# Kernel optimization log

Measured on AMD Instinct MI355X. Metric: run time of the kernel, lower is better.

Reference implementation:

```python
import jax, jax.numpy as jnp
import numpy as np

CHUNK = 1024
HEAD_DIM = 128

def setup_inputs() -> dict:
    key = jax.random.key(0)
    k1, k2, k3 = jax.random.split(key, 3)
    B, H, S, D = 2, 16, 4096, HEAD_DIM
    q = jax.random.normal(k1, (B, H, S, D), dtype=jnp.float32)
    k = jax.random.normal(k2, (B, H, S, D), dtype=jnp.float32)
    v = jax.random.normal(k3, (B, H, S, D), dtype=jnp.float32)
    return {"q": q, "k": k, "v": v}

def reference(q, k, v):
    # Faithful to the torch module INCLUDING its masking bug: for every chunk
    # the triu mask uses diagonal=1 in chunk-local coordinates, so chunk-local
    # query row i attends only keys j<=i, i.e. only the first CHUNK keys matter.
    B, H, S, D = q.shape
    scale = D ** (-0.5)
    n = S // CHUNK
    qc = q.reshape(B, H, n, CHUNK, D)           # [B,H,n,C,D]
    kc = k[:, :, :CHUNK, :]                      # [B,H,C,D]
    vc = v[:, :, :CHUNK, :]                      # [B,H,C,D]
    scores = jnp.einsum('bhnid,bhjd->bhnij', qc, kc) * scale  # [B,H,n,C,C]
    mask = jnp.triu(jnp.ones((CHUNK, CHUNK), dtype=bool), 1)   # j > i masked
    scores = jnp.where(mask, -jnp.inf, scores)
    probs = jax.nn.softmax(scores, axis=-1)
    out = jnp.einsum('bhnij,bhjd->bhnid', probs, vc)
    return out.reshape(B, H, S, D)
```

## Files before the change

kernel.cpp:

```cpp
#include <hip/hip_runtime.h>


typedef __attribute__((ext_vector_type(8))) short bfrag_t;
typedef __attribute__((ext_vector_type(16))) float f32x16;
typedef unsigned short u16;
typedef unsigned int   u32;

#define SEQ     4096
#define SCHUNK  1024
#define HD      128
#define NTILE   16
#define TILE_E  8192

__device__ __forceinline__ u16 f2bf(float f) {
    union { float f; unsigned u; } x; x.f = f;
    unsigned r = x.u + 0x7fffu + ((x.u >> 16) & 1u);
    return (u16)(r >> 16);
}

__global__ __launch_bounds__(256)
void mea_prep(const float* __restrict__ kg, const float* __restrict__ vg,
              u16* __restrict__ wsK, u16* __restrict__ wsV)
{
    const int tid  = threadIdx.x;
    const int tile = blockIdx.x;
    const int bh = tile >> 4, kt = tile & 15;
    const long gsrc = (long)bh * SEQ * HD + (long)kt * 64 * HD;
    const long gdst = (long)tile * TILE_E;

#pragma unroll
    for (int i = 0; i < 4; ++i) {
        int oid = i * 256 + tid;
        int j = oid >> 4, s = oid & 15;
        const float* kp = kg + gsrc + j * HD + s * 8;
        float4 a = *(const float4*)kp;
        float4 b = *(const float4*)(kp + 4);
        bfrag_t f;
        f[0]=f2bf(a.x); f[1]=f2bf(a.y); f[2]=f2bf(a.z); f[3]=f2bf(a.w);
        f[4]=f2bf(b.x); f[5]=f2bf(b.y); f[6]=f2bf(b.z); f[7]=f2bf(b.w);
        *(bfrag_t*)(wsK + gdst + j * 128 + ((s ^ (j & 15)) * 8)) = f;
    }
#pragma unroll
    for (int i = 0; i < 4; ++i) {
        int oid = i * 256 + tid;
        int jo = oid >> 7, d = oid & 127;
        const float* vp = vg + gsrc + jo * 8 * HD + d;
        bfrag_t f;
#pragma unroll
        for (int jj = 0; jj < 8; ++jj) f[jj] = f2bf(vp[jj * HD]);
        int d2 = d >> 1;
        int S  = (jo + ((d & 1) << 3)) ^ (d2 & 15);
        *(bfrag_t*)(wsV + gdst + d2 * 128 + S * 8) = f;
    }
}

__device__ __forceinline__ void gll16(const u16* g, u16* l) {
    __builtin_amdgcn_global_load_lds((const __attribute__((address_space(1))) u32*)g,
                                     (__attribute__((address_space(3))) u32*)l, 16, 0, 0);
}

__device__ __forceinline__ float tsum16(const f32x16& p) {
    float a0 = (p[0] + p[1]) + (p[2] + p[3]);
    float a1 = (p[4] + p[5]) + (p[6] + p[7]);
    float a2 = (p[8] + p[9]) + (p[10] + p[11]);
    float a3 = (p[12] + p[13]) + (p[14] + p[15]);
    return (a0 + a1) + (a2 + a3);
}

__global__ __launch_bounds__(256, 2)
void mea_main(const float* __restrict__ qg, const u16* __restrict__ wsK,
              const u16* __restrict__ wsV, float* __restrict__ og)
{
    __shared__ __align__(16) u16 K_s[2][TILE_E];
    __shared__ __align__(16) u16 V_s[2][TILE_E];

    const int tid  = threadIdx.x;
    const int lane = tid & 63;
    const int wv   = tid >> 6;
    const int c31  = lane & 31;
    const int hi   = lane >> 5;

    const int x   = blockIdx.x & 7;
    const int idx = blockIdx.x >> 3;
    const int p   = idx >> 2;
    const int bh  = x * 4 + (idx & 3);

    const long bhrow = (long)bh * SEQ + (long)wv * SCHUNK;
    const u16* Kb = wsK + (long)bh * NTILE * TILE_E;
    const u16* Vb = wsV + (long)bh * NTILE * TILE_E;
    const int so   = wv * 2048 + lane * 8;
    const int ldsb = wv * 2048;
    const float qs = 0.12751723f;

#pragma unroll
    for (int c = 0; c < 4; ++c) {
        gll16(Kb + so + c * 512, &K_s[0][ldsb + c * 512]);
        gll16(Vb + so + c * 512, &V_s[0][ldsb + c * 512]);
    }

    int cur = 0;
    for (int seg = 0; seg < 2; ++seg) {
        const int qt  = seg ? p : (31 - p);
        const int nt  = (qt >> 1) + 1;
        const int par = qt & 1;
        const long rowbase = bhrow + (long)qt * 32;

        bfrag_t qf[8];
        {
            const float* qp = qg + (rowbase + c31) * HD + hi * 8;
#pragma unroll
            for (int ks = 0; ks < 8; ++ks) {
                float4 a = *(const float4*)(qp + ks * 16);
                float4 b = *(const float4*)(qp + ks * 16 + 4);
                bfrag_t f;
                f[0]=f2bf(a.x*qs); f[1]=f2bf(a.y*qs); f[2]=f2bf(a.z*qs); f[3]=f2bf(a.w*qs);
                f[4]=f2bf(b.x*qs); f[5]=f2bf(b.y*qs); f[6]=f2bf(b.z*qs); f[7]=f2bf(b.w*qs);
                qf[ks] = f;
            }
        }

        f32x16 oacc[4];
#pragma unroll
        for (int d = 0; d < 4; ++d)
#pragma unroll
            for (int i = 0; i < 16; ++i) oacc[d][i] = 0.f;
        float lsum = 0.f;

        for (int kt = 0; kt < nt; ++kt) {
            __syncthreads();

            if (kt + 1 < nt) {
                const long tb = (long)(kt + 1) * TILE_E;
#pragma unroll
                for (int c = 0; c < 4; ++c) {
                    gll16(Kb + tb + so + c * 512, &K_s[cur ^ 1][ldsb + c * 512]);
                    gll16(Vb + tb + so + c * 512, &V_s[cur ^ 1][ldsb + c * 512]);
                }
            } else if (seg == 0) {
#pragma unroll
                for (int c = 0; c < 4; ++c) {
                    gll16(Kb + so + c * 512, &K_s[cur ^ 1][ldsb + c * 512]);
                    gll16(Vb + so + c * 512, &V_s[cur ^ 1][ldsb + c * 512]);
                }
            }

            const bool diag = (kt == nt - 1);
            const bool do1  = !(diag && par == 0);
            bfrag_t pfrag[4];

            {
                f32x16 s;
#pragma unroll
                for (int i = 0; i < 16; ++i) s[i] = 0.f;
                const u16* krow = &K_s[cur][c31 * 128];
#pragma unroll
                for (int ks = 0; ks < 8; ++ks) {
                    int slot = (ks * 2 + hi) ^ (c31 & 15);
                    bfrag_t kf = *(const bfrag_t*)(krow + slot * 8);
                    s = __builtin_amdgcn_mfma_f32_32x32x16_bf16(kf, qf[ks], s, 0, 0, 0);
                }
                if (diag && par == 0) {
#pragma unroll
                    for (int r = 0; r < 16; ++r) {
                        int crow = (r & 3) + 8 * (r >> 2) + 4 * hi;
                        if (crow > c31) s[r] = -1e30f;
                    }
                }
#pragma unroll
                for (int r = 0; r < 16; ++r) s[r] = exp2f(s[r]);
                lsum += tsum16(s);
                u32 W[8];
#pragma unroll
                for (int t2 = 0; t2 < 8; ++t2)
                    asm("v_cvt_pk_bf16_f32 %0, %1, %2"
                        : "=v"(W[t2]) : "v"(s[2 * t2]), "v"(s[2 * t2 + 1]));
#pragma unroll
                for (int u2 = 0; u2 < 2; ++u2) {
                    u32 x0 = W[4 * u2 + 0], y0 = W[4 * u2 + 2];
                    u32 x1 = W[4 * u2 + 1], y1 = W[4 * u2 + 3];
                    asm("v_permlane32_swap_b32 %0, %1" : "+v"(x0), "+v"(y0));
                    asm("v_permlane32_swap_b32 %0, %1" : "+v"(x1), "+v"(y1));
                    union { u32 w[4]; bfrag_t f; } cvt;
                    cvt.w[0] = x0; cvt.w[1] = x1; cvt.w[2] = y0; cvt.w[3] = y1;
                    pfrag[u2] = cvt.f;
                }
            }
            if (do1) {
                f32x16 s;
#pragma unroll
                for (int i = 0; i < 16; ++i) s[i] = 0.f;
                const u16* krow = &K_s[cur][(32 + c31) * 128];
#pragma unroll
                for (int ks = 0; ks < 8; ++ks) {
                    int slot = (ks * 2 + hi) ^ (c31 & 15);
                    bfrag_t kf = *(const bfrag_t*)(krow + slot * 8);
                    s = __builtin_amdgcn_mfma_f32_32x32x16_bf16(kf, qf[ks], s, 0, 0, 0);
                }
                if (diag) {
#pragma unroll
                    for (int r = 0; r < 16; ++r) {
                        int crow = (r & 3) + 8 * (r >> 2) + 4 * hi;
                        if (crow > c31) s[r] = -1e30f;
                    }
                }
#pragma unroll
                for (int r = 0; r < 16; ++r) s[r] = exp2f(s[r]);
                lsum += tsum16(s);
                u32 W[8];
#pragma unroll
                for (int t2 = 0; t2 < 8; ++t2)
                    asm("v_cvt_pk_bf16_f32 %0, %1, %2"
                        : "=v"(W[t2]) : "v"(s[2 * t2]), "v"(s[2 * t2 + 1]));
#pragma unroll
                for (int u2 = 0; u2 < 2; ++u2) {
                    u32 x0 = W[4 * u2 + 0], y0 = W[4 * u2 + 2];
                    u32 x1 = W[4 * u2 + 1], y1 = W[4 * u2 + 3];
                    asm("v_permlane32_swap_b32 %0, %1" : "+v"(x0), "+v"(y0));
                    asm("v_permlane32_swap_b32 %0, %1" : "+v"(x1), "+v"(y1));
                    union { u32 w[4]; bfrag_t f; } cvt;
                    cvt.w[0] = x0; cvt.w[1] = x1; cvt.w[2] = y0; cvt.w[3] = y1;
                    pfrag[2 + u2] = cvt.f;
                }
            }

#pragma unroll
            for (int dg = 0; dg < 4; ++dg) {
                const int d  = dg * 32 + c31;
                const int d2 = d >> 1;
                const u16* vrow = &V_s[cur][d2 * 128];
#pragma unroll
                for (int jsl = 0; jsl < 2; ++jsl) {
                    int S = ((jsl * 2 + hi) + ((d & 1) << 3)) ^ (d2 & 15);
                    bfrag_t vf = *(const bfrag_t*)(vrow + S * 8);
                    oacc[dg] = __builtin_amdgcn_mfma_f32_32x32x16_bf16(vf, pfrag[jsl], oacc[dg], 0, 0, 0);
                }
            }
            if (do1) {
#pragma unroll
                for (int dg = 0; dg < 4; ++dg) {
                    const int d  = dg * 32 + c31;
                    const int d2 = d >> 1;
                    const u16* vrow = &V_s[cur][d2 * 128];
#pragma unroll
                    for (int jsl = 2; jsl < 4; ++jsl) {
                        int S = ((jsl * 2 + hi) + ((d & 1) << 3)) ^ (d2 & 15);
                        bfrag_t vf = *(const bfrag_t*)(vrow + S * 8);
                        oacc[dg] = __builtin_amdgcn_mfma_f32_32x32x16_bf16(vf, pfrag[jsl], oacc[dg], 0, 0, 0);
                    }
                }
            }

            cur ^= 1;
        }

        lsum += __shfl_xor(lsum, 32);
        float inv = 1.f / lsum;
#pragma unroll
        for (int dg = 0; dg < 4; ++dg) {
#pragma unroll
            for (int rq = 0; rq < 4; ++rq) {
                float4 v;
                v.x = oacc[dg][rq * 4 + 0] * inv;
                v.y = oacc[dg][rq * 4 + 1] * inv;
                v.z = oacc[dg][rq * 4 + 2] * inv;
                v.w = oacc[dg][rq * 4 + 3] * inv;
                *(float4*)(og + (rowbase + c31) * HD + dg * 32 + rq * 8 + hi * 4) = v;
            }
        }
    }
}

extern "C" void kernel_launch(void* const* d_in, const int* in_sizes, int n_in,
                              void* d_out, int out_size, void* d_ws, size_t ws_size,
                              hipStream_t stream)
{
    (void)in_sizes; (void)n_in; (void)out_size; (void)ws_size;
    const float* q = (const float*)d_in[0];
    const float* k = (const float*)d_in[1];
    const float* v = (const float*)d_in[2];
    float* o = (float*)d_out;
    u16* wsK = (u16*)d_ws;
    u16* wsV = wsK + (size_t)32 * NTILE * TILE_E;
    mea_prep<<<dim3(512), dim3(256), 0, stream>>>(k, v, wsK, wsV);
    mea_main<<<dim3(512), dim3(256), 0, stream>>>(q, wsK, wsV, o);
}
```

Before: 76.98 us.

## Use 512-thread blocks with two waves per chunk sharing K/V tiles, add MFMA priority

Blocks now hold 8 waves: four chunks, each split into two 32-row query halves. The two halves share each 64-key K/V tile staged in LDS, so every tile load serves twice as many query rows and global-to-LDS traffic per output drops. The grid is halved and query tiles become 64 rows, with the causal diagonal handled per half. s_setprio raises wave priority around the MFMA sections, and the softmax-convert code is factored into a helper. Larger blocks and fewer workgroups may reduce occupancy flexibility and tail balance.

Result: no change. 75.85 us (-1.5%).

```diff
diff --git a/kernel.cpp b/kernel.cpp
--- a/kernel.cpp
+++ b/kernel.cpp
@@ -67,7 +67,28 @@
     return (a0 + a1) + (a2 + a3);
 }
 
-__global__ __launch_bounds__(256, 2)
+__device__ __forceinline__ void sm_cvt(f32x16& s, float& lsum, bfrag_t* pf) {
+#pragma unroll
+    for (int r = 0; r < 16; ++r) s[r] = exp2f(s[r]);
+    lsum += tsum16(s);
+    u32 W[8];
+#pragma unroll
+    for (int t2 = 0; t2 < 8; ++t2)
+        asm("v_cvt_pk_bf16_f32 %0, %1, %2"
+            : "=v"(W[t2]) : "v"(s[2 * t2]), "v"(s[2 * t2 + 1]));
+#pragma unroll
+    for (int u2 = 0; u2 < 2; ++u2) {
+        u32 x0 = W[4 * u2 + 0], y0 = W[4 * u2 + 2];
+        u32 x1 = W[4 * u2 + 1], y1 = W[4 * u2 + 3];
+        asm("v_permlane32_swap_b32 %0, %1" : "+v"(x0), "+v"(y0));
+        asm("v_permlane32_swap_b32 %0, %1" : "+v"(x1), "+v"(y1));
+        union { u32 w[4]; bfrag_t f; } cvt;
+        cvt.w[0] = x0; cvt.w[1] = x1; cvt.w[2] = y0; cvt.w[3] = y1;
+        pf[u2] = cvt.f;
+    }
+}
+
+__global__ __launch_bounds__(512, 2)
 void mea_main(const float* __restrict__ qg, const u16* __restrict__ wsK,
               const u16* __restrict__ wsV, float* __restrict__ og)
 {
@@ -79,31 +100,32 @@
     const int wv   = tid >> 6;
     const int c31  = lane & 31;
     const int hi   = lane >> 5;
+    const int ch   = wv & 3;
+    const int h    = wv >> 2;
 
     const int x   = blockIdx.x & 7;
     const int idx = blockIdx.x >> 3;
+    const int bh  = x * 4 + (idx & 3);
     const int p   = idx >> 2;
-    const int bh  = x * 4 + (idx & 3);
-
-    const long bhrow = (long)bh * SEQ + (long)wv * SCHUNK;
+
+    const long bhrow = (long)bh * SEQ + (long)ch * SCHUNK + (long)h * 32;
     const u16* Kb = wsK + (long)bh * NTILE * TILE_E;
     const u16* Vb = wsV + (long)bh * NTILE * TILE_E;
-    const int so   = wv * 2048 + lane * 8;
-    const int ldsb = wv * 2048;
+    const int so   = wv * 1024 + lane * 8;
+    const int ldsb = wv * 1024;
     const float qs = 0.12751723f;
 
 #pragma unroll
-    for (int c = 0; c < 4; ++c) {
+    for (int c = 0; c < 2; ++c) {
         gll16(Kb + so + c * 512, &K_s[0][ldsb + c * 512]);
         gll16(Vb + so + c * 512, &V_s[0][ldsb + c * 512]);
     }
 
     int cur = 0;
     for (int seg = 0; seg < 2; ++seg) {
-        const int qt  = seg ? p : (31 - p);
-        const int nt  = (qt >> 1) + 1;
-        const int par = qt & 1;
-        const long rowbase = bhrow + (long)qt * 32;
+        const int qt = seg ? p : (15 - p);
+        const int nt = qt + 1;
+        const long rowbase = bhrow + (long)qt * 64;
 
         bfrag_t qf[8];
         {
@@ -132,70 +154,57 @@
             if (kt + 1 < nt) {
                 const long tb = (long)(kt + 1) * TILE_E;
 #pragma unroll
-                for (int c = 0; c < 4; ++c) {
+                for (int c = 0; c < 2; ++c) {
                     gll16(Kb + tb + so + c * 512, &K_s[cur ^ 1][ldsb + c * 512]);
                     gll16(Vb + tb + so + c * 512, &V_s[cur ^ 1][ldsb + c * 512]);
                 }
             } else if (seg == 0) {
 #pragma unroll
-                for (int c = 0; c < 4; ++c) {
+                for (int c = 0; c < 2; ++c) {
                     gll16(Kb + so + c * 512, &K_s[cur ^ 1][ldsb + c * 512]);
                     gll16(Vb + so + c * 512, &V_s[cur ^ 1][ldsb + c * 512]);
                 }
             }
 
             const bool diag = (kt == nt - 1);
-            const bool do1  = !(diag && par == 0);
-            bfrag_t pfrag[4];
+            const bool do1  = !(diag && h == 0);
+            bfrag_t pfA[2], pfB[2];
 
             {
                 f32x16 s;
 #pragma unroll
                 for (int i = 0; i < 16; ++i) s[i] = 0.f;
                 const u16* krow = &K_s[cur][c31 * 128];
+                __builtin_amdgcn_s_setprio(1);
 #pragma unroll
                 for (int ks = 0; ks < 8; ++ks) {
                     int slot = (ks * 2 + hi) ^ (c31 & 15);
                     bfrag_t kf = *(const bfrag_t*)(krow + slot * 8);
                     s = __builtin_amdgcn_mfma_f32_32x32x16_bf16(kf, qf[ks], s, 0, 0, 0);
                 }
-                if (diag && par == 0) {
+                __builtin_amdgcn_s_setprio(0);
+                if (diag && h == 0) {
 #pragma unroll
                     for (int r = 0; r < 16; ++r) {
                         int crow = (r & 3) + 8 * (r >> 2) + 4 * hi;
                         if (crow > c31) s[r] = -1e30f;
                     }
                 }
-#pragma unroll
-                for (int r = 0; r < 16; ++r) s[r] = exp2f(s[r]);
-                lsum += tsum16(s);
-                u32 W[8];
-#pragma unroll
-                for (int t2 = 0; t2 < 8; ++t2)
-                    asm("v_cvt_pk_bf16_f32 %0, %1, %2"
-                        : "=v"(W[t2]) : "v"(s[2 * t2]), "v"(s[2 * t2 + 1]));
-#pragma unroll
-                for (int u2 = 0; u2 < 2; ++u2) {
-                    u32 x0 = W[4 * u2 + 0], y0 = W[4 * u2 + 2];
-                    u32 x1 = W[4 * u2 + 1], y1 = W[4 * u2 + 3];
-                    asm("v_permlane32_swap_b32 %0, %1" : "+v"(x0), "+v"(y0));
-                    asm("v_permlane32_swap_b32 %0, %1" : "+v"(x1), "+v"(y1));
-                    union { u32 w[4]; bfrag_t f; } cvt;
-                    cvt.w[0] = x0; cvt.w[1] = x1; cvt.w[2] = y0; cvt.w[3] = y1;
-                    pfrag[u2] = cvt.f;
-                }
+                sm_cvt(s, lsum, pfA);
             }
             if (do1) {
                 f32x16 s;
 #pragma unroll
                 for (int i = 0; i < 16; ++i) s[i] = 0.f;
                 const u16* krow = &K_s[cur][(32 + c31) * 128];
+                __builtin_amdgcn_s_setprio(1);
 #pragma unroll
                 for (int ks = 0; ks < 8; ++ks) {
                     int slot = (ks * 2 + hi) ^ (c31 & 15);
                     bfrag_t kf = *(const bfrag_t*)(krow + slot * 8);
                     s = __builtin_amdgcn_mfma_f32_32x32x16_bf16(kf, qf[ks], s, 0, 0, 0);
                 }
+                __builtin_amdgcn_s_setprio(0);
                 if (diag) {
 #pragma unroll
                     for (int r = 0; r < 16; ++r) {
@@ -203,26 +212,10 @@
                         if (crow > c31) s[r] = -1e30f;
                     }
                 }
-#pragma unroll
-                for (int r = 0; r < 16; ++r) s[r] = exp2f(s[r]);
-                lsum += tsum16(s);
-                u32 W[8];
-#pragma unroll
-                for (int t2 = 0; t2 < 8; ++t2)
-                    asm("v_cvt_pk_bf16_f32 %0, %1, %2"
-                        : "=v"(W[t2]) : "v"(s[2 * t2]), "v"(s[2 * t2 + 1]));
-#pragma unroll
-                for (int u2 = 0; u2 < 2; ++u2) {
-                    u32 x0 = W[4 * u2 + 0], y0 = W[4 * u2 + 2];
-                    u32 x1 = W[4 * u2 + 1], y1 = W[4 * u2 + 3];
-                    asm("v_permlane32_swap_b32 %0, %1" : "+v"(x0), "+v"(y0));
-                    asm("v_permlane32_swap_b32 %0, %1" : "+v"(x1), "+v"(y1));
-                    union { u32 w[4]; bfrag_t f; } cvt;
-                    cvt.w[0] = x0; cvt.w[1] = x1; cvt.w[2] = y0; cvt.w[3] = y1;
-                    pfrag[2 + u2] = cvt.f;
-                }
-            }
-
+                sm_cvt(s, lsum, pfB);
+            }
+
+            __builtin_amdgcn_s_setprio(1);
 #pragma unroll
             for (int dg = 0; dg < 4; ++dg) {
                 const int d  = dg * 32 + c31;
@@ -232,23 +225,18 @@
                 for (int jsl = 0; jsl < 2; ++jsl) {
                     int S = ((jsl * 2 + hi) + ((d & 1) << 3)) ^ (d2 & 15);
                     bfrag_t vf = *(const bfrag_t*)(vrow + S * 8);
-                    oacc[dg] = __builtin_amdgcn_mfma_f32_32x32x16_bf16(vf, pfrag[jsl], oacc[dg], 0, 0, 0);
-                }
-            }
-            if (do1) {
-#pragma unroll
-                for (int dg = 0; dg < 4; ++dg) {
-                    const int d  = dg * 32 + c31;
-                    const int d2 = d >> 1;
-                    const u16* vrow = &V_s[cur][d2 * 128];
-#pragma unroll
-                    for (int jsl = 2; jsl < 4; ++jsl) {
-                        int S = ((jsl * 2 + hi) + ((d & 1) << 3)) ^ (d2 & 15);
+                    oacc[dg] = __builtin_amdgcn_mfma_f32_32x32x16_bf16(vf, pfA[jsl], oacc[dg], 0, 0, 0);
+                }
+                if (do1) {
+#pragma unroll
+                    for (int jsl = 0; jsl < 2; ++jsl) {
+                        int S = ((jsl + 2) * 2 + hi + ((d & 1) << 3)) ^ (d2 & 15);
                         bfrag_t vf = *(const bfrag_t*)(vrow + S * 8);
-                        oacc[dg] = __builtin_amdgcn_mfma_f32_32x32x16_bf16(vf, pfrag[jsl], oacc[dg], 0, 0, 0);
+                        oacc[dg] = __builtin_amdgcn_mfma_f32_32x32x16_bf16(vf, pfB[jsl], oacc[dg], 0, 0, 0);
                     }
                 }
             }
+            __builtin_amdgcn_s_setprio(0);
 
             cur ^= 1;
         }
@@ -282,5 +270,5 @@
     u16* wsK = (u16*)d_ws;
     u16* wsV = wsK + (size_t)32 * NTILE * TILE_E;
     mea_prep<<<dim3(512), dim3(256), 0, stream>>>(k, v, wsK, wsV);
-    mea_main<<<dim3(512), dim3(256), 0, stream>>>(q, wsK, wsV, o);
-}
+    mea_main<<<dim3(256), dim3(512), 0, stream>>>(q, wsK, wsV, o);
+}
```
